# Kernel optimization log

Hardware: AMD Instinct MI355X
Metric: run time of the kernel (lower is better)

## Reference

```python
import jax, jax.numpy as jnp
import numpy as np

B, S, D, H, E = 2, 2048, 1024, 4096, 8
TOP_K = 2


def setup_inputs() -> dict:
    key = jax.random.key(0)
    ks = jax.random.split(key, 5)
    scale = 0.02
    return {
        "x": jax.random.normal(ks[0], (B, S, D), dtype=jnp.float32),
        "gate_w": jax.random.normal(ks[1], (D, E), dtype=jnp.float32) * scale,
        "gate_b": jnp.zeros((E,), dtype=jnp.float32),
        "w1": jax.random.normal(ks[2], (E, D, H), dtype=jnp.float32) * scale,
        "b1": jnp.zeros((E, H), dtype=jnp.float32),
        "w2": jax.random.normal(ks[3], (E, H, D), dtype=jnp.float32) * scale,
        "b2": jnp.zeros((E, D), dtype=jnp.float32),
    }


def reference(x, gate_w, gate_b, w1, b1, w2, b2):
    # Gating: softmax over experts, then top-k selection. [B,S,E]
    gate_logits = jnp.einsum("bsd,de->bse", x, gate_w) + gate_b
    gate_weights = jax.nn.softmax(gate_logits, axis=-1)
    topk_values, topk_indices = jax.lax.top_k(gate_weights, TOP_K)  # [B,S,K]

    # Dense all-expert FFN (faithful to source, which runs every expert on every token).
    hidden = jax.nn.relu(jnp.einsum("bsd,edh->bseh", x, w1) + b1)  # [B,S,E,H]
    expert_out = jnp.einsum("bseh,ehd->bsed", hidden, w2) + b2      # [B,S,E,D]

    # Gather top-k expert outputs per token and combine with gate weights.
    sel = jnp.take_along_axis(expert_out, topk_indices[..., None], axis=2)  # [B,S,K,D]
    return jnp.sum(topk_values[..., None] * sel, axis=2)  # [B,S,D]
```

## Files before the change

### kernel.cpp

```cpp
#include <hip/hip_runtime.h>
#include <stdint.h>

#define BB 2
#define SS 2048
#define DD 1024
#define HH 4096
#define EE 8
#define NTOK (BB*SS)
#define NPAIR (NTOK*2)

#define BM 128
#define BM2 64
#define BN 128
#define BK 64
#define KSPLIT 2

typedef float f32x4 __attribute__((ext_vector_type(4)));
typedef __bf16 bf16x8 __attribute__((ext_vector_type(8)));
typedef short s16x4 __attribute__((ext_vector_type(4)));
typedef short s16x8 __attribute__((ext_vector_type(8)));

__device__ __forceinline__ unsigned short f2bf(float f) {
    union { float f; uint32_t u; } v; v.f = f;
    return (unsigned short)((v.u + 0x7FFFu + ((v.u >> 16) & 1u)) >> 16);
}
__device__ __forceinline__ float bf2f(unsigned short u) {
    union { uint32_t u; float f; } v; v.u = ((uint32_t)u) << 16; return v.f;
}

__device__ __forceinline__ void gload16(const void* g, void* l) {
    __builtin_amdgcn_global_load_lds(
        (const __attribute__((address_space(1))) unsigned int*)g,
        (__attribute__((address_space(3))) unsigned int*)l, 16, 0, 0);
}

__global__ __launch_bounds__(256) void gate_kernel(
    const float* __restrict__ x, const float* __restrict__ gw,
    const float* __restrict__ gb,
    int* __restrict__ cnt, int* __restrict__ tok, int* __restrict__ pid,
    int* __restrict__ etok, float* __restrict__ wtok,
    unsigned short* __restrict__ xb)
{
    int wave = threadIdx.x >> 6;
    int lane = threadIdx.x & 63;
    int t = blockIdx.x * 4 + wave;
    if (t >= NTOK) return;

    float acc[EE];
#pragma unroll
    for (int e = 0; e < EE; ++e) acc[e] = 0.f;

    const float* xr = x + (size_t)t * DD;
    unsigned short* xo = xb + (size_t)t * DD;
    for (int d = lane; d < DD; d += 64) {
        float xv = xr[d];
        xo[d] = f2bf(xv);
        const float* g = gw + (size_t)d * EE;
#pragma unroll
        for (int e = 0; e < EE; ++e) acc[e] += xv * g[e];
    }
#pragma unroll
    for (int e = 0; e < EE; ++e) {
#pragma unroll
        for (int off = 32; off >= 1; off >>= 1)
            acc[e] += __shfl_xor(acc[e], off);
    }
    if (lane == 0) {
        float lg[EE];
        float m = -1e30f;
#pragma unroll
        for (int e = 0; e < EE; ++e) { lg[e] = acc[e] + gb[e]; m = fmaxf(m, lg[e]); }
        float s = 0.f;
#pragma unroll
        for (int e = 0; e < EE; ++e) { lg[e] = expf(lg[e] - m); s += lg[e]; }
        float inv = 1.f / s;
        int e0 = 0; float v0 = lg[0];
#pragma unroll
        for (int e = 1; e < EE; ++e) if (lg[e] > v0) { v0 = lg[e]; e0 = e; }
        int e1 = -1; float v1 = -1.f;
#pragma unroll
        for (int e = 0; e < EE; ++e) if (e != e0 && lg[e] > v1) { v1 = lg[e]; e1 = e; }

        int p0 = atomicAdd(&cnt[e0], 1);
        tok[e0 * NTOK + p0] = t; pid[e0 * NTOK + p0] = 2 * t;
        int p1 = atomicAdd(&cnt[e1], 1);
        tok[e1 * NTOK + p1] = t; pid[e1 * NTOK + p1] = 2 * t + 1;
        etok[2 * t] = e0;     wtok[2 * t] = v0 * inv;
        etok[2 * t + 1] = e1; wtok[2 * t + 1] = v1 * inv;
    }
}

__global__ __launch_bounds__(256) void transpose_cvt_kernel(
    const float* __restrict__ in, unsigned short* __restrict__ out, int R, int C)
{
    __shared__ float t[64][65];
    const int e = blockIdx.z;
    const int r0 = blockIdx.y * 64;
    const int c0 = blockIdx.x * 64;
    const float* src = in + (size_t)e * R * C;
    unsigned short* dst = out + (size_t)e * R * C;
    const int tid = threadIdx.x;
    const int lr = tid >> 4;
    const int lc = (tid & 15) * 4;
#pragma unroll
    for (int p = 0; p < 4; ++p) {
        int row = p * 16 + lr;
        const float4 v = *(const float4*)(src + (size_t)(r0 + row) * C + c0 + lc);
        t[row][lc]     = v.x; t[row][lc + 1] = v.y;
        t[row][lc + 2] = v.z; t[row][lc + 3] = v.w;
    }
    __syncthreads();
#pragma unroll
    for (int p = 0; p < 4; ++p) {
        int crow = p * 16 + lr;
        s16x4 b;
#pragma unroll
        for (int j = 0; j < 4; ++j) b[j] = (short)f2bf(t[lc + j][crow]);
        *(s16x4*)(dst + (size_t)(c0 + crow) * R + r0 + lc) = b;
    }
}

__global__ __launch_bounds__(256, 4) void ffn1_kernel(
    const unsigned short* __restrict__ xb, const unsigned short* __restrict__ w1t,
    const float* __restrict__ b1,
    const int* __restrict__ cnt, const int* __restrict__ tok,
    const int* __restrict__ pid,
    unsigned short* __restrict__ hid, int ebase)
{
    const int le = blockIdx.z;
    const int e = ebase + le;
    const int mt = blockIdx.y;
    const int nt = blockIdx.x;
    const int Me = cnt[e];
    if (mt * BM >= Me) return;

    __shared__ unsigned short As[BM][BK];
    __shared__ unsigned short Bs[BN][BK];
    __shared__ int tl[BM];

    const int tid = threadIdx.x;
    if (tid < BM) {
        int p = mt * BM + tid;
        tl[tid] = (p < Me) ? tok[e * NTOK + p] : 0;
    }
    __syncthreads();

    const int lane = tid & 63;
    const int wv = tid >> 6;
    const int wr = wv >> 1, wc = wv & 1;

    const int srow = lane >> 3;
    const int scol = ((lane & 7) ^ srow) * 8;

    const unsigned short* aSrc[4];
#pragma unroll
    for (int i = 0; i < 4; ++i)
        aSrc[i] = xb + (size_t)tl[wv * 32 + i * 8 + srow] * DD + scol;
    const unsigned short* bE = w1t + (size_t)le * DD * HH;
    const unsigned short* bSrc[4];
#pragma unroll
    for (int i = 0; i < 4; ++i)
        bSrc[i] = bE + (size_t)(nt * BN + wv * 32 + i * 8 + srow) * DD + scol;

    f32x4 acc[4][4];
#pragma unroll
    for (int m = 0; m < 4; ++m)
#pragma unroll
        for (int n = 0; n < 4; ++n)
#pragma unroll
            for (int q = 0; q < 4; ++q) acc[m][n][q] = 0.f;

    for (int t = 0; t < DD / BK; ++t) {
        const int k0 = t * BK;
#pragma unroll
        for (int i = 0; i < 4; ++i) gload16(aSrc[i] + k0, &As[wv * 32 + i * 8][0]);
#pragma unroll
        for (int i = 0; i < 4; ++i) gload16(bSrc[i] + k0, &Bs[wv * 32 + i * 8][0]);
        __syncthreads();
#pragma unroll
        for (int ks = 0; ks < BK; ks += 32) {
            bf16x8 af[4], bfr[4];
            const int g = (ks >> 3) + (lane >> 4);
#pragma unroll
            for (int m = 0; m < 4; ++m) {
                int ar = wr * 64 + m * 16 + (lane & 15);
                af[m] = *(const bf16x8*)&As[ar][(g ^ (ar & 7)) * 8];
            }
#pragma unroll
            for (int n = 0; n < 4; ++n) {
                int br = wc * 64 + n * 16 + (lane & 15);
                bfr[n] = *(const bf16x8*)&Bs[br][(g ^ (br & 7)) * 8];
            }
#pragma unroll
            for (int m = 0; m < 4; ++m)
#pragma unroll
                for (int n = 0; n < 4; ++n)
                    acc[m][n] = __builtin_amdgcn_mfma_f32_16x16x32_bf16(af[m], bfr[n], acc[m][n], 0, 0, 0);
        }
        __syncthreads();
    }

    const int nbase = nt * BN;
#pragma unroll
    for (int m = 0; m < 4; ++m) {
#pragma unroll
        for (int q = 0; q < 4; ++q) {
            int rloc = wr * 64 + m * 16 + (lane >> 4) * 4 + q;
            int p = mt * BM + rloc;
            if (p < Me) {
                int pp = pid[e * NTOK + p];
                unsigned short* dst = hid + (size_t)pp * HH;
#pragma unroll
                for (int n = 0; n < 4; ++n) {
                    int ng = nbase + wc * 64 + n * 16 + (lane & 15);
                    float h = acc[m][n][q] + b1[(size_t)e * HH + ng];
                    dst[ng] = f2bf(fmaxf(h, 0.f));
                }
            }
        }
    }
}

__global__ __launch_bounds__(256, 5) void ffn2_kernel(
    const unsigned short* __restrict__ hid, const unsigned short* __restrict__ w2t,
    const int* __restrict__ cnt, const int* __restrict__ pid,
    unsigned short* __restrict__ chunks, int ebase)
{
    const int le = blockIdx.z >> 1;
    const int kc = blockIdx.z & 1;
    const int e = ebase + le;
    const int mt = blockIdx.y;
    const int nt = blockIdx.x;
    const int Me = cnt[e];
    if (mt * BM2 >= Me) return;

    __shared__ unsigned short As[BM2][BK];
    __shared__ unsigned short Bs[BN][BK];
    __shared__ int pl[BM2];

    const int tid = threadIdx.x;
    if (tid < BM2) {
        int p = mt * BM2 + tid;
        pl[tid] = (p < Me) ? pid[e * NTOK + p] : 0;
    }
    __syncthreads();

    const int lane = tid & 63;
    const int wv = tid >> 6;

    const int srow = lane >> 3;
    const int scol = ((lane & 7) ^ srow) * 8;
    const int kbase = kc * (HH / KSPLIT);

    const unsigned short* aSrc[2];
#pragma unroll
    for (int i = 0; i < 2; ++i)
        aSrc[i] = hid + (size_t)pl[wv * 16 + i * 8 + srow] * HH + kbase + scol;
    const unsigned short* bE = w2t + (size_t)le * DD * HH;
    const unsigned short* bSrc[4];
#pragma unroll
    for (int i = 0; i < 4; ++i)
        bSrc[i] = bE + (size_t)(nt * BN + wv * 32 + i * 8 + srow) * HH + kbase + scol;

    f32x4 acc[4][2];
#pragma unroll
    for (int m = 0; m < 4; ++m)
#pragma unroll
        for (int n = 0; n < 2; ++n)
#pragma unroll
            for (int q = 0; q < 4; ++q) acc[m][n][q] = 0.f;

    for (int t = 0; t < (HH / KSPLIT) / BK; ++t) {
        const int k0 = t * BK;
#pragma unroll
        for (int i = 0; i < 2; ++i) gload16(aSrc[i] + k0, &As[wv * 16 + i * 8][0]);
#pragma unroll
        for (int i = 0; i < 4; ++i) gload16(bSrc[i] + k0, &Bs[wv * 32 + i * 8][0]);
        __syncthreads();
#pragma unroll
        for (int ks = 0; ks < BK; ks += 32) {
            bf16x8 af[4], bfr[2];
            const int g = (ks >> 3) + (lane >> 4);
#pragma unroll
            for (int m = 0; m < 4; ++m) {
                int ar = m * 16 + (lane & 15);
                af[m] = *(const bf16x8*)&As[ar][(g ^ (ar & 7)) * 8];
            }
#pragma unroll
            for (int n = 0; n < 2; ++n) {
                int br = wv * 32 + n * 16 + (lane & 15);
                bfr[n] = *(const bf16x8*)&Bs[br][(g ^ (br & 7)) * 8];
            }
#pragma unroll
            for (int m = 0; m < 4; ++m)
#pragma unroll
                for (int n = 0; n < 2; ++n)
                    acc[m][n] = __builtin_amdgcn_mfma_f32_16x16x32_bf16(af[m], bfr[n], acc[m][n], 0, 0, 0);
        }
        __syncthreads();
    }

    const int nbase = nt * BN;
    unsigned short* cbase = chunks + (size_t)kc * NPAIR * DD;
#pragma unroll
    for (int m = 0; m < 4; ++m) {
#pragma unroll
        for (int q = 0; q < 4; ++q) {
            int rloc = m * 16 + (lane >> 4) * 4 + q;
            int p = mt * BM2 + rloc;
            if (p < Me) {
                int pp = pl[rloc];
                unsigned short* dst = cbase + (size_t)pp * DD;
#pragma unroll
                for (int n = 0; n < 2; ++n) {
                    int ng = nbase + wv * 32 + n * 16 + (lane & 15);
                    dst[ng] = f2bf(acc[m][n][q]);
                }
            }
        }
    }
}

__global__ __launch_bounds__(256) void combine_kernel(
    const unsigned short* __restrict__ chunks, const float* __restrict__ b2,
    const int* __restrict__ etok, const float* __restrict__ wtok,
    float* __restrict__ out)
{
    const int t = blockIdx.x;
    const int d0 = threadIdx.x * 4;
    f32x4 s;
    s[0] = s[1] = s[2] = s[3] = 0.f;
#pragma unroll
    for (int k = 0; k < 2; ++k) {
        const int pair = 2 * t + k;
        const float w = wtok[pair];
        const int e = etok[pair];
        s16x4 c0 = *(const s16x4*)(chunks + (size_t)pair * DD + d0);
        s16x4 c1 = *(const s16x4*)(chunks + (size_t)(NPAIR + pair) * DD + d0);
        const float4 bb = *(const float4*)(b2 + (size_t)e * DD + d0);
        s[0] += w * (bf2f((unsigned short)c0[0]) + bf2f((unsigned short)c1[0]) + bb.x);
        s[1] += w * (bf2f((unsigned short)c0[1]) + bf2f((unsigned short)c1[1]) + bb.y);
        s[2] += w * (bf2f((unsigned short)c0[2]) + bf2f((unsigned short)c1[2]) + bb.z);
        s[3] += w * (bf2f((unsigned short)c0[3]) + bf2f((unsigned short)c1[3]) + bb.w);
    }
    *(f32x4*)(out + (size_t)t * DD + d0) = s;
}

extern "C" void kernel_launch(void* const* d_in, const int* in_sizes, int n_in,
                              void* d_out, int out_size, void* d_ws, size_t ws_size,
                              hipStream_t stream) {
    const float* x   = (const float*)d_in[0];
    const float* gw  = (const float*)d_in[1];
    const float* gb  = (const float*)d_in[2];
    const float* w1  = (const float*)d_in[3];
    const float* b1  = (const float*)d_in[4];
    const float* w2  = (const float*)d_in[5];
    const float* b2  = (const float*)d_in[6];
    float* out = (float*)d_out;

    char* ws = (char*)d_ws;
    size_t off = 0;
    int*   cnt  = (int*)(ws + off);   off += 256;
    int*   tok  = (int*)(ws + off);   off += (size_t)4 * EE * NTOK;
    int*   pid  = (int*)(ws + off);   off += (size_t)4 * EE * NTOK;
    int*   etok = (int*)(ws + off);   off += (size_t)4 * NPAIR;
    float* wtok = (float*)(ws + off); off += (size_t)4 * NPAIR;
    unsigned short* xb     = (unsigned short*)(ws + off); off += (size_t)NTOK * DD * 2;
    unsigned short* hid    = (unsigned short*)(ws + off); off += (size_t)NPAIR * HH * 2;
    unsigned short* wt     = (unsigned short*)(ws + off); off += (size_t)(EE / 2) * DD * HH * 2;
    unsigned short* chunks = (unsigned short*)(ws + off); off += (size_t)KSPLIT * NPAIR * DD * 2;

    hipMemsetAsync(cnt, 0, 256, stream);

    gate_kernel<<<NTOK / 4, 256, 0, stream>>>(x, gw, gb, cnt, tok, pid, etok, wtok, xb);

    for (int h = 0; h < 2; ++h) {
        const int e0 = h * 4;
        transpose_cvt_kernel<<<dim3(HH / 64, DD / 64, 4), 256, 0, stream>>>(
            w1 + (size_t)e0 * DD * HH, wt, DD, HH);
        ffn1_kernel<<<dim3(HH / BN, NTOK / BM, 4), 256, 0, stream>>>(
            xb, wt, b1, cnt, tok, pid, hid, e0);
    }
    for (int h = 0; h < 2; ++h) {
        const int e0 = h * 4;
        transpose_cvt_kernel<<<dim3(DD / 64, HH / 64, 4), 256, 0, stream>>>(
            w2 + (size_t)e0 * HH * DD, wt, HH, DD);
        ffn2_kernel<<<dim3(DD / BN, NTOK / BM2, 4 * KSPLIT), 256, 0, stream>>>(
            hid, wt, cnt, pid, chunks, e0);
    }

    combine_kernel<<<NTOK, 256, 0, stream>>>(chunks, b2, etok, wtok, out);
}
```

Before: 645.9 us.

## Fuse combine into ffn2 via atomics, drop K-split, process all experts per launch

```diff
diff --git a/kernel.cpp b/kernel.cpp
--- a/kernel.cpp
+++ b/kernel.cpp
@@ -13,7 +13,6 @@
 #define BM2 64
 #define BN 128
 #define BK 64
-#define KSPLIT 2
 
 typedef float f32x4 __attribute__((ext_vector_type(4)));
 typedef __bf16 bf16x8 __attribute__((ext_vector_type(8)));
@@ -24,9 +23,6 @@
     union { float f; uint32_t u; } v; v.f = f;
     return (unsigned short)((v.u + 0x7FFFu + ((v.u >> 16) & 1u)) >> 16);
 }
-__device__ __forceinline__ float bf2f(unsigned short u) {
-    union { uint32_t u; float f; } v; v.u = ((uint32_t)u) << 16; return v.f;
-}
 
 __device__ __forceinline__ void gload16(const void* g, void* l) {
     __builtin_amdgcn_global_load_lds(
@@ -34,10 +30,9 @@
         (__attribute__((address_space(3))) unsigned int*)l, 16, 0, 0);
 }
 
-__global__ __launch_bounds__(256) void gate_kernel(
+__global__ __launch_bounds__(256) void gate_compute(
     const float* __restrict__ x, const float* __restrict__ gw,
     const float* __restrict__ gb,
-    int* __restrict__ cnt, int* __restrict__ tok, int* __restrict__ pid,
     int* __restrict__ etok, float* __restrict__ wtok,
     unsigned short* __restrict__ xb)
 {
@@ -81,13 +76,27 @@
 #pragma unroll
         for (int e = 0; e < EE; ++e) if (e != e0 && lg[e] > v1) { v1 = lg[e]; e1 = e; }
 
-        int p0 = atomicAdd(&cnt[e0], 1);
-        tok[e0 * NTOK + p0] = t; pid[e0 * NTOK + p0] = 2 * t;
-        int p1 = atomicAdd(&cnt[e1], 1);
-        tok[e1 * NTOK + p1] = t; pid[e1 * NTOK + p1] = 2 * t + 1;
         etok[2 * t] = e0;     wtok[2 * t] = v0 * inv;
         etok[2 * t + 1] = e1; wtok[2 * t + 1] = v1 * inv;
     }
+}
+
+__global__ __launch_bounds__(1024) void scatter_kernel(
+    const int* __restrict__ etok,
+    int* __restrict__ cnt, int* __restrict__ tok, int* __restrict__ pid)
+{
+    __shared__ int lcnt[EE];
+    const int tid = threadIdx.x;
+    if (tid < EE) lcnt[tid] = 0;
+    __syncthreads();
+    for (int p = tid; p < NPAIR; p += 1024) {
+        int e = etok[p];
+        int r = atomicAdd(&lcnt[e], 1);
+        tok[e * NTOK + r] = p >> 1;
+        pid[e * NTOK + r] = p;
+    }
+    __syncthreads();
+    if (tid < EE) cnt[tid] = lcnt[tid];
 }
 
 __global__ __launch_bounds__(256) void transpose_cvt_kernel(
@@ -125,10 +134,9 @@
     const float* __restrict__ b1,
     const int* __restrict__ cnt, const int* __restrict__ tok,
     const int* __restrict__ pid,
-    unsigned short* __restrict__ hid, int ebase)
-{
-    const int le = blockIdx.z;
-    const int e = ebase + le;
+    unsigned short* __restrict__ hid)
+{
+    const int e = blockIdx.z;
     const int mt = blockIdx.y;
     const int nt = blockIdx.x;
     const int Me = cnt[e];
@@ -156,7 +164,7 @@
 #pragma unroll
     for (int i = 0; i < 4; ++i)
         aSrc[i] = xb + (size_t)tl[wv * 32 + i * 8 + srow] * DD + scol;
-    const unsigned short* bE = w1t + (size_t)le * DD * HH;
+    const unsigned short* bE = w1t + (size_t)e * DD * HH;
     const unsigned short* bSrc[4];
 #pragma unroll
     for (int i = 0; i < 4; ++i)
@@ -223,12 +231,12 @@
 
 __global__ __launch_bounds__(256, 5) void ffn2_kernel(
     const unsigned short* __restrict__ hid, const unsigned short* __restrict__ w2t,
+    const float* __restrict__ b2,
     const int* __restrict__ cnt, const int* __restrict__ pid,
-    unsigned short* __restrict__ chunks, int ebase)
-{
-    const int le = blockIdx.z >> 1;
-    const int kc = blockIdx.z & 1;
-    const int e = ebase + le;
+    const float* __restrict__ wtok,
+    float* __restrict__ out)
+{
+    const int e = blockIdx.z;
     const int mt = blockIdx.y;
     const int nt = blockIdx.x;
     const int Me = cnt[e];
@@ -250,17 +258,16 @@
 
     const int srow = lane >> 3;
     const int scol = ((lane & 7) ^ srow) * 8;
-    const int kbase = kc * (HH / KSPLIT);
 
     const unsigned short* aSrc[2];
 #pragma unroll
     for (int i = 0; i < 2; ++i)
-        aSrc[i] = hid + (size_t)pl[wv * 16 + i * 8 + srow] * HH + kbase + scol;
-    const unsigned short* bE = w2t + (size_t)le * DD * HH;
+        aSrc[i] = hid + (size_t)pl[wv * 16 + i * 8 + srow] * HH + scol;
+    const unsigned short* bE = w2t + (size_t)e * DD * HH;
     const unsigned short* bSrc[4];
 #pragma unroll
     for (int i = 0; i < 4; ++i)
-        bSrc[i] = bE + (size_t)(nt * BN + wv * 32 + i * 8 + srow) * HH + kbase + scol;
+        bSrc[i] = bE + (size_t)(nt * BN + wv * 32 + i * 8 + srow) * HH + scol;
 
     f32x4 acc[4][2];
 #pragma unroll
@@ -270,7 +277,7 @@
 #pragma unroll
             for (int q = 0; q < 4; ++q) acc[m][n][q] = 0.f;
 
-    for (int t = 0; t < (HH / KSPLIT) / BK; ++t) {
+    for (int t = 0; t < HH / BK; ++t) {
         const int k0 = t * BK;
 #pragma unroll
         for (int i = 0; i < 2; ++i) gload16(aSrc[i] + k0, &As[wv * 16 + i * 8][0]);
@@ -301,7 +308,6 @@
     }
 
     const int nbase = nt * BN;
-    unsigned short* cbase = chunks + (size_t)kc * NPAIR * DD;
 #pragma unroll
     for (int m = 0; m < 4; ++m) {
 #pragma unroll
@@ -310,40 +316,17 @@
             int p = mt * BM2 + rloc;
             if (p < Me) {
                 int pp = pl[rloc];
-                unsigned short* dst = cbase + (size_t)pp * DD;
+                int t = pp >> 1;
+                float wvv = wtok[pp];
+                float* dst = out + (size_t)t * DD;
 #pragma unroll
                 for (int n = 0; n < 2; ++n) {
                     int ng = nbase + wv * 32 + n * 16 + (lane & 15);
-                    dst[ng] = f2bf(acc[m][n][q]);
+                    atomicAdd(&dst[ng], wvv * (acc[m][n][q] + b2[(size_t)e * DD + ng]));
                 }
             }
         }
     }
-}
-
-__global__ __launch_bounds__(256) void combine_kernel(
-    const unsigned short* __restrict__ chunks, const float* __restrict__ b2,
-    const int* __restrict__ etok, const float* __restrict__ wtok,
-    float* __restrict__ out)
-{
-    const int t = blockIdx.x;
-    const int d0 = threadIdx.x * 4;
-    f32x4 s;
-    s[0] = s[1] = s[2] = s[3] = 0.f;
-#pragma unroll
-    for (int k = 0; k < 2; ++k) {
-        const int pair = 2 * t + k;
-        const float w = wtok[pair];
-        const int e = etok[pair];
-        s16x4 c0 = *(const s16x4*)(chunks + (size_t)pair * DD + d0);
-        s16x4 c1 = *(const s16x4*)(chunks + (size_t)(NPAIR + pair) * DD + d0);
-        const float4 bb = *(const float4*)(b2 + (size_t)e * DD + d0);
-        s[0] += w * (bf2f((unsigned short)c0[0]) + bf2f((unsigned short)c1[0]) + bb.x);
-        s[1] += w * (bf2f((unsigned short)c0[1]) + bf2f((unsigned short)c1[1]) + bb.y);
-        s[2] += w * (bf2f((unsigned short)c0[2]) + bf2f((unsigned short)c1[2]) + bb.z);
-        s[3] += w * (bf2f((unsigned short)c0[3]) + bf2f((unsigned short)c1[3]) + bb.w);
-    }
-    *(f32x4*)(out + (size_t)t * DD + d0) = s;
 }
 
 extern "C" void kernel_launch(void* const* d_in, const int* in_sizes, int n_in,
@@ -365,29 +348,20 @@
     int*   pid  = (int*)(ws + off);   off += (size_t)4 * EE * NTOK;
     int*   etok = (int*)(ws + off);   off += (size_t)4 * NPAIR;
     float* wtok = (float*)(ws + off); off += (size_t)4 * NPAIR;
-    unsigned short* xb     = (unsigned short*)(ws + off); off += (size_t)NTOK * DD * 2;
-    unsigned short* hid    = (unsigned short*)(ws + off); off += (size_t)NPAIR * HH * 2;
-    unsigned short* wt     = (unsigned short*)(ws + off); off += (size_t)(EE / 2) * DD * HH * 2;
-    unsigned short* chunks = (unsigned short*)(ws + off); off += (size_t)KSPLIT * NPAIR * DD * 2;
-
-    hipMemsetAsync(cnt, 0, 256, stream);
-
-    gate_kernel<<<NTOK / 4, 256, 0, stream>>>(x, gw, gb, cnt, tok, pid, etok, wtok, xb);
-
-    for (int h = 0; h < 2; ++h) {
-        const int e0 = h * 4;
-        transpose_cvt_kernel<<<dim3(HH / 64, DD / 64, 4), 256, 0, stream>>>(
-            w1 + (size_t)e0 * DD * HH, wt, DD, HH);
-        ffn1_kernel<<<dim3(HH / BN, NTOK / BM, 4), 256, 0, stream>>>(
-            xb, wt, b1, cnt, tok, pid, hid, e0);
-    }
-    for (int h = 0; h < 2; ++h) {
-        const int e0 = h * 4;
-        transpose_cvt_kernel<<<dim3(DD / 64, HH / 64, 4), 256, 0, stream>>>(
-            w2 + (size_t)e0 * HH * DD, wt, HH, DD);
-        ffn2_kernel<<<dim3(DD / BN, NTOK / BM2, 4 * KSPLIT), 256, 0, stream>>>(
-            hid, wt, cnt, pid, chunks, e0);
-    }
-
-    combine_kernel<<<NTOK, 256, 0, stream>>>(chunks, b2, etok, wtok, out);
-}
+    unsigned short* xb  = (unsigned short*)(ws + off); off += (size_t)NTOK * DD * 2;
+    unsigned short* hid = (unsigned short*)(ws + off); off += (size_t)NPAIR * HH * 2;
+    unsigned short* wt  = (unsigned short*)(ws + off); off += (size_t)EE * DD * HH * 2;
+
+    hipMemsetAsync(out, 0, (size_t)out_size * sizeof(float), stream);
+
+    gate_compute<<<NTOK / 4, 256, 0, stream>>>(x, gw, gb, etok, wtok, xb);
+    scatter_kernel<<<1, 1024, 0, stream>>>(etok, cnt, tok, pid);
+
+    transpose_cvt_kernel<<<dim3(HH / 64, DD / 64, EE), 256, 0, stream>>>(w1, wt, DD, HH);
+    ffn1_kernel<<<dim3(HH / BN, NTOK / BM, EE), 256, 0, stream>>>(
+        xb, wt, b1, cnt, tok, pid, hid);
+
+    transpose_cvt_kernel<<<dim3(DD / 64, HH / 64, EE), 256, 0, stream>>>(w2, wt, HH, DD);
+    ffn2_kernel<<<dim3(DD / BN, NTOK / BM2, EE), 256, 0, stream>>>(
+        hid, wt, b2, cnt, pid, wtok, out);
+}
```

Result: faster. 557.6 us (-13.7%).
